# Performance work log

Hardware: AMD Instinct MI355X
Metric: run time of the kernel (lower is better)

Reference implementation:

```python
import jax, jax.numpy as jnp
import numpy as np

N = 4096          # num_nodes
F = 64            # node_features
H = 128           # hidden_dim
NH = 4            # num_heads
HD = H // NH      # per-head dim = 32
L = 3             # num_layers
C = 7             # num_classes
EDGE_P = 0.004    # ~16 avg degree


def setup_inputs() -> dict:
    key = jax.random.key(0)
    ks = jax.random.split(key, 20)
    g = lambda k, shape, fan_in: jax.random.normal(k, shape, jnp.float32) / np.sqrt(fan_in)
    x = jax.random.normal(ks[0], (N, F), jnp.float32)
    adj = (jax.random.uniform(ks[1], (N, N)) < EDGE_P).astype(jnp.float32)
    return {
        "x": x,
        "adj": adj,
        "enc_W": g(ks[2], (F, H), F), "enc_b": jnp.zeros((H,), jnp.float32),
        "gcn_W": g(ks[3], (L, H, H), H), "gcn_b": jnp.zeros((L, H), jnp.float32),
        "attn_W": g(ks[4], (L, NH, H, HD), H), "attn_Wb": jnp.zeros((L, NH, HD), jnp.float32),
        "attn_a": g(ks[5], (L, NH, 2 * HD), 2 * HD), "attn_ab": jnp.zeros((L, NH), jnp.float32),
        "cls_W1": g(ks[6], (H, H // 2), H), "cls_b1": jnp.zeros((H // 2,), jnp.float32),
        "cls_W2": g(ks[7], (H // 2, C), H // 2), "cls_b2": jnp.zeros((C,), jnp.float32),
        "con_W1": g(ks[8], (H, H // 2), H), "con_b1": jnp.zeros((H // 2,), jnp.float32),
        "con_W2": g(ks[9], (H // 2, 1), H // 2), "con_b2": jnp.zeros((1,), jnp.float32),
    }


def _normalize_adj(adj):
    a = adj + jnp.eye(adj.shape[0], dtype=adj.dtype)
    dinv = jnp.sum(a, axis=1) ** -0.5
    return dinv[:, None] * a * dinv[None, :]


def _gcn(h, adj_norm, W, b):
    support = adj_norm @ h                      # [N,H]
    return jax.nn.relu(support @ W + b)         # dropout=0 (eval)


def _attention(h, edge_mask, W, Wb, a, ab):
    # h:[N,H], W:[NH,H,HD], a:[NH,2*HD]; per-pair score = Linear(concat(h_i,h_j))
    hh = jnp.einsum('nf,hfd->hnd', h, W) + Wb[:, None, :]     # [NH,N,HD]
    a_src, a_dst = a[:, :HD], a[:, HD:]
    s_src = jnp.einsum('hnd,hd->hn', hh, a_src)               # [NH,N]
    s_dst = jnp.einsum('hnd,hd->hn', hh, a_dst)               # [NH,N]
    scores = s_src[:, :, None] + s_dst[:, None, :] + ab[:, None, None]
    # original uses literal 0.0 (NOT -inf) for non-edges before softmax
    scores = jnp.where(edge_mask[None, :, :], scores, 0.0)    # [NH,N,N]
    probs = jax.nn.softmax(scores, axis=-1)
    out = jnp.einsum('hij,hjd->hid', probs, hh)               # [NH,N,HD]
    return out.transpose(1, 0, 2).reshape(h.shape[0], NH * HD)


def reference(x, adj, enc_W, enc_b, gcn_W, gcn_b, attn_W, attn_Wb, attn_a, attn_ab,
              cls_W1, cls_b1, cls_W2, cls_b2, con_W1, con_b1, con_W2, con_b2):
    h = jax.nn.relu(x @ enc_W + enc_b)          # node encoder (dropout=0)
    adj_norm = _normalize_adj(adj)
    edge_mask = adj > 0
    for i in range(L):
        h_gcn = _gcn(h, adj_norm, gcn_W[i], gcn_b[i])
        h_attn = _attention(h, edge_mask, attn_W[i], attn_Wb[i], attn_a[i], attn_ab[i])
        h = jax.nn.relu(h_gcn + h_attn)
    node_logits = jax.nn.relu(h @ cls_W1 + cls_b1) @ cls_W2 + cls_b2
    h_mean = jnp.mean(h, axis=0, keepdims=True)
    contagion = jax.nn.relu(h_mean @ con_W1 + con_b1) @ con_W2 + con_b2
    return (node_logits, h, contagion)
```

## Files before the change

kernel.cpp:

```cpp
#include <hip/hip_runtime.h>

typedef unsigned short u16;
typedef unsigned int u32;

#define N 4096
#define F 64
#define H 128
#define NH 4
#define HD 32
#define EMAX 64

__device__ float g_hA[N * H];
__device__ float g_hB[N * H];
__device__ float g_hhA[N * H];
__device__ float g_hhB[N * H];
__device__ u16   g_cols[N * EMAX];
__device__ int   g_deg[N];
__device__ float g_dinv[N];
__device__ float g_ssrcA[N * NH];
__device__ float g_ssrcB[N * NH];
__device__ float g_sdstA[N * NH];
__device__ float g_sdstB[N * NH];
__device__ float g_part[3][32][H];
__device__ float g_hpart[32][H];

__global__ void k_csr(const float* __restrict__ adj) {
  __shared__ int cnt;
  int row = blockIdx.x;
  if (threadIdx.x == 0) cnt = 0;
  if (row == 0) {
    float* pz = &g_part[0][0][0];
    for (int i = threadIdx.x; i < 3 * 32 * H; i += 256) pz[i] = 0.f;
    float* hz = &g_hpart[0][0];
    for (int i = threadIdx.x; i < 32 * H; i += 256) hz[i] = 0.f;
  }
  __syncthreads();
  int base = threadIdx.x * 16;
  const float4* p = reinterpret_cast<const float4*>(adj + (size_t)row * N + base);
  float4 q0 = p[0], q1 = p[1], q2 = p[2], q3 = p[3];
  float vals[16] = {q0.x, q0.y, q0.z, q0.w, q1.x, q1.y, q1.z, q1.w,
                    q2.x, q2.y, q2.z, q2.w, q3.x, q3.y, q3.z, q3.w};
#pragma unroll
  for (int t = 0; t < 16; ++t)
    if (vals[t] != 0.f) {
      int pos = atomicAdd(&cnt, 1);
      if (pos < EMAX) g_cols[row * EMAX + pos] = (u16)(base + t);
    }
  __syncthreads();
  if (threadIdx.x == 0) {
    g_deg[row] = cnt < EMAX ? cnt : EMAX;
    g_dinv[row] = 1.0f / sqrtf((float)(cnt + 1));
  }
}

__device__ __forceinline__ void agg4(int i0, int tid, const float* __restrict__ h,
                                     const float* __restrict__ hhin,
                                     const float* __restrict__ ssrc_in,
                                     const float* __restrict__ sdst_in,
                                     int l, const float* __restrict__ abv,
                                     int (&jl)[4][EMAX], float (&dv)[4][EMAX],
                                     float (&sdl)[4][EMAX * NH],
                                     float& outa0, float& outa1,
                                     float& sup0, float& sup1) {
  int c = tid & 127, rg = tid >> 7, hc = c >> 5;
  int darr[4];
#pragma unroll
  for (int r = 0; r < 4; ++r) darr[r] = g_deg[i0 + r];
#pragma unroll
  for (int r = 0; r < 4; ++r) {
    const u16* cl = g_cols + (size_t)(i0 + r) * EMAX;
    for (int e = tid; e < darr[r]; e += 256) {
      int j = cl[e];
      jl[r][e] = j;
      dv[r][e] = g_dinv[j];
    }
  }
  __syncthreads();
#pragma unroll
  for (int r = 0; r < 4; ++r)
    for (int idx = tid; idx < darr[r] * NH; idx += 256)
      sdl[r][idx] = sdst_in[jl[r][idx >> 2] * NH + (idx & 3)];
  __syncthreads();

  float sumc = 0.f;
  const float* part = &g_part[l][0][0];
#pragma unroll
  for (int s = 0; s < 32; ++s) sumc += part[s * H + c];
  float ab = abv[hc];

  float oa[2], sp[2];
#pragma unroll
  for (int rr = 0; rr < 2; ++rr) {
    int r = rg * 2 + rr;
    int i = i0 + r, dd = darr[r];
    float ssrc = ssrc_in[i * NH + hc];
    float M = -INFINITY;
    for (int e = 0; e < dd; ++e) M = fmaxf(M, sdl[r][e * NH + hc]);
    float mv = fmaxf(0.f, ssrc + ab + M);
    float em = expf(-mv);
    float base = ssrc + ab - mv;
    float aA = 0.f, aT = 0.f, aG = 0.f, S = 0.f;
    int e = 0;
    for (; e + 2 <= dd; e += 2) {
      int j0 = jl[r][e], j1 = jl[r][e + 1];
      float q0 = hhin[j0 * H + c], q1 = hhin[j1 * H + c];
      float p0 = h[j0 * H + c], p1 = h[j1 * H + c];
      float w0 = expf(base + sdl[r][e * NH + hc]);
      float w1 = expf(base + sdl[r][(e + 1) * NH + hc]);
      aA = fmaf(w0, q0, aA); aA = fmaf(w1, q1, aA);
      aT += q0 + q1;
      aG = fmaf(dv[r][e], p0, aG); aG = fmaf(dv[r][e + 1], p1, aG);
      S += w0 + w1;
    }
    for (; e < dd; ++e) {
      int j = jl[r][e];
      float w = expf(base + sdl[r][e * NH + hc]);
      float q = hhin[j * H + c];
      aA = fmaf(w, q, aA);
      aT += q;
      aG = fmaf(dv[r][e], h[j * H + c], aG);
      S += w;
    }
    float Z = S + em * (float)(N - dd);
    oa[rr] = (aA + em * (sumc - aT)) / Z;
    float di = g_dinv[i];
    sp[rr] = di * (aG + di * h[i * H + c]);
  }
  outa0 = oa[0]; outa1 = oa[1]; sup0 = sp[0]; sup1 = sp[1];
}

__device__ __forceinline__ void proj4(int i0, int tid, const float (&hrowT)[H][4],
                                      const float* __restrict__ aW,
                                      const float* __restrict__ aWb,
                                      const float* __restrict__ aa, int lp,
                                      float* __restrict__ hhout,
                                      float* __restrict__ ssrc_out,
                                      float* __restrict__ sdst_out) {
  int c = tid & 127, rg = tid >> 7, hc = c >> 5, dc = c & 31;
  float b = aWb[hc * HD + dc];
  float p0 = b, p1 = b;
  for (int f = 0; f < H; ++f) {
    float w = aW[(hc * H + f) * HD + dc];
    float2 hv = *reinterpret_cast<const float2*>(&hrowT[f][rg * 2]);
    p0 = fmaf(hv.x, w, p0);
    p1 = fmaf(hv.y, w, p1);
  }
  int r0 = i0 + rg * 2, r1 = r0 + 1;
  hhout[r0 * H + c] = p0;
  hhout[r1 * H + c] = p1;
  const float* ap = aa + hc * 2 * HD;
  float as = ap[dc], ad = ap[HD + dc];
  float ss0 = p0 * as, ss1 = p1 * as, sd0 = p0 * ad, sd1 = p1 * ad;
#pragma unroll
  for (int m = 16; m >= 1; m >>= 1) {
    ss0 += __shfl_xor(ss0, m, 64); ss1 += __shfl_xor(ss1, m, 64);
    sd0 += __shfl_xor(sd0, m, 64); sd1 += __shfl_xor(sd1, m, 64);
  }
  if (dc == 0) {
    ssrc_out[r0 * NH + hc] = ss0; ssrc_out[r1 * NH + hc] = ss1;
    sdst_out[r0 * NH + hc] = sd0; sdst_out[r1 * NH + hc] = sd1;
  }
  atomicAdd(&g_part[lp][r0 & 31][c], p0);
  atomicAdd(&g_part[lp][r1 & 31][c], p1);
}

__global__ void k_enc_proj(const float* __restrict__ x, const float* __restrict__ eW,
                           const float* __restrict__ eb, const float* __restrict__ aW,
                           const float* __restrict__ aWb, const float* __restrict__ aa) {
  __shared__ float xT[F][4];
  __shared__ float hrowT[H][4];
  int i0 = blockIdx.x * 4, tid = threadIdx.x;
  int c = tid & 127, rg = tid >> 7;
  {
    int r = tid >> 6, k = tid & 63;
    xT[k][r] = x[(i0 + r) * F + k];
  }
  __syncthreads();
  float b = eb[c];
  float e0 = b, e1 = b;
  for (int k = 0; k < F; ++k) {
    float w = eW[k * H + c];
    float2 xv = *reinterpret_cast<const float2*>(&xT[k][rg * 2]);
    e0 = fmaf(xv.x, w, e0);
    e1 = fmaf(xv.y, w, e1);
  }
  e0 = fmaxf(e0, 0.f); e1 = fmaxf(e1, 0.f);
  int r0 = i0 + rg * 2, r1 = r0 + 1;
  g_hA[r0 * H + c] = e0; g_hA[r1 * H + c] = e1;
  hrowT[c][rg * 2] = e0; hrowT[c][rg * 2 + 1] = e1;
  __syncthreads();
  proj4(i0, tid, hrowT, aW, aWb, aa, 0, g_hhA, g_ssrcA, g_sdstA);
}

__global__ void k_acp(int pp, int l, const float* __restrict__ gW,
                      const float* __restrict__ gb, const float* __restrict__ aW,
                      const float* __restrict__ aWb, const float* __restrict__ aa,
                      const float* __restrict__ abv) {
  const float* h    = pp ? g_hB : g_hA;
  float*       hout = pp ? g_hA : g_hB;
  const float* hhin = pp ? g_hhB : g_hhA;
  float*       hhout= pp ? g_hhA : g_hhB;
  const float* ssin = pp ? g_ssrcB : g_ssrcA;
  float*       ssout= pp ? g_ssrcA : g_ssrcB;
  const float* sdin = pp ? g_sdstB : g_sdstA;
  float*       sdout= pp ? g_sdstA : g_sdstB;
  __shared__ int   jl[4][EMAX];
  __shared__ float dv[4][EMAX];
  __shared__ float sdl[4][EMAX * NH];
  __shared__ float srowT[H][4];
  __shared__ float hrowT[H][4];
  int i0 = blockIdx.x * 4, tid = threadIdx.x;
  int c = tid & 127, rg = tid >> 7;

  float oa0, oa1, sp0, sp1;
  agg4(i0, tid, h, hhin, ssin, sdin, l, abv, jl, dv, sdl, oa0, oa1, sp0, sp1);
  srowT[c][rg * 2] = sp0; srowT[c][rg * 2 + 1] = sp1;
  __syncthreads();

  float b = gb[c];
  float a0 = b, a1 = b;
  for (int f = 0; f < H; ++f) {
    float w = gW[f * H + c];
    float2 sv = *reinterpret_cast<const float2*>(&srowT[f][rg * 2]);
    a0 = fmaf(sv.x, w, a0);
    a1 = fmaf(sv.y, w, a1);
  }
  float g0 = fmaxf(fmaxf(a0, 0.f) + oa0, 0.f);
  float g1 = fmaxf(fmaxf(a1, 0.f) + oa1, 0.f);
  int r0 = i0 + rg * 2, r1 = r0 + 1;
  hout[r0 * H + c] = g0; hout[r1 * H + c] = g1;
  hrowT[c][rg * 2] = g0; hrowT[c][rg * 2 + 1] = g1;
  __syncthreads();

  proj4(i0, tid, hrowT, aW, aWb, aa, l + 1, hhout, ssout, sdout);
}

__global__ void k_acc(const float* __restrict__ abv, const float* __restrict__ gW,
                      const float* __restrict__ gb,
                      const float* __restrict__ W1, const float* __restrict__ b1,
                      const float* __restrict__ W2, const float* __restrict__ b2,
                      float* __restrict__ out, float* __restrict__ outh) {
  __shared__ int   jl[4][EMAX];
  __shared__ float dv[4][EMAX];
  __shared__ float sdl[4][EMAX * NH];
  __shared__ float srowT[H][4];
  __shared__ float hrowT[H][4];
  __shared__ float tl[4][64];
  int i0 = blockIdx.x * 4, tid = threadIdx.x;
  int c = tid & 127, rg = tid >> 7;

  float oa0, oa1, sp0, sp1;
  agg4(i0, tid, g_hA, g_hhA, g_ssrcA, g_sdstA, 2, abv, jl, dv, sdl, oa0, oa1, sp0, sp1);
  srowT[c][rg * 2] = sp0; srowT[c][rg * 2 + 1] = sp1;
  __syncthreads();

  float b = gb[c];
  float a0 = b, a1 = b;
  for (int f = 0; f < H; ++f) {
    float w = gW[f * H + c];
    float2 sv = *reinterpret_cast<const float2*>(&srowT[f][rg * 2]);
    a0 = fmaf(sv.x, w, a0);
    a1 = fmaf(sv.y, w, a1);
  }
  float g0 = fmaxf(fmaxf(a0, 0.f) + oa0, 0.f);
  float g1 = fmaxf(fmaxf(a1, 0.f) + oa1, 0.f);
  int r0 = i0 + rg * 2, r1 = r0 + 1;
  outh[r0 * H + c] = g0; outh[r1 * H + c] = g1;
  hrowT[c][rg * 2] = g0; hrowT[c][rg * 2 + 1] = g1;
  atomicAdd(&g_hpart[r0 & 31][c], g0);
  atomicAdd(&g_hpart[r1 & 31][c], g1);
  __syncthreads();

  int u = tid & 63, rr4 = tid >> 6;
  float a2 = b1[u];
  for (int f = 0; f < H; ++f) a2 = fmaf(hrowT[f][rr4], W1[f * 64 + u], a2);
  tl[rr4][u] = fmaxf(a2, 0.f);
  __syncthreads();
  if (tid < 28) {
    int r = tid / 7, j = tid - r * 7;
    float p = b2[j];
    for (int v = 0; v < 64; ++v) p = fmaf(tl[r][v], W2[v * 7 + j], p);
    out[(i0 + r) * 7 + j] = p;
  }
}

__global__ void k_contagion(const float* __restrict__ W1, const float* __restrict__ b1,
                            const float* __restrict__ W2, const float* __restrict__ b2,
                            float* __restrict__ out) {
  __shared__ float hm[H];
  __shared__ float tl[64];
  int u = threadIdx.x;
#pragma unroll
  for (int q = 0; q < 2; ++q) {
    int col = u + q * 64;
    float s = 0.f;
#pragma unroll
    for (int sl = 0; sl < 32; ++sl) s += g_hpart[sl][col];
    hm[col] = s * (1.0f / 4096.0f);
  }
  __syncthreads();
  float acc = b1[u];
  for (int f = 0; f < H; ++f) acc = fmaf(hm[f], W1[f * 64 + u], acc);
  tl[u] = fmaxf(acc, 0.f);
  __syncthreads();
  if (u == 0) {
    float p = b2[0];
    for (int v = 0; v < 64; ++v) p = fmaf(tl[v], W2[v], p);
    out[0] = p;
  }
}

extern "C" void kernel_launch(void* const* d_in, const int* in_sizes, int n_in,
                              void* d_out, int out_size, void* d_ws, size_t ws_size,
                              hipStream_t stream) {
  const float* x       = (const float*)d_in[0];
  const float* adj     = (const float*)d_in[1];
  const float* enc_W   = (const float*)d_in[2];
  const float* enc_b   = (const float*)d_in[3];
  const float* gcn_W   = (const float*)d_in[4];
  const float* gcn_b   = (const float*)d_in[5];
  const float* attn_W  = (const float*)d_in[6];
  const float* attn_Wb = (const float*)d_in[7];
  const float* attn_a  = (const float*)d_in[8];
  const float* attn_ab = (const float*)d_in[9];
  const float* cls_W1  = (const float*)d_in[10];
  const float* cls_b1  = (const float*)d_in[11];
  const float* cls_W2  = (const float*)d_in[12];
  const float* cls_b2  = (const float*)d_in[13];
  const float* con_W1  = (const float*)d_in[14];
  const float* con_b1  = (const float*)d_in[15];
  const float* con_W2  = (const float*)d_in[16];
  const float* con_b2  = (const float*)d_in[17];
  (void)in_sizes; (void)n_in; (void)d_ws; (void)ws_size; (void)out_size;

  float* out = (float*)d_out;
  float* outh = out + (size_t)N * 7;
  float* outc = out + (size_t)N * 7 + (size_t)N * H;

  k_csr<<<N, 256, 0, stream>>>(adj);
  k_enc_proj<<<N / 4, 256, 0, stream>>>(x, enc_W, enc_b, attn_W, attn_Wb, attn_a);
  k_acp<<<N / 4, 256, 0, stream>>>(0, 0, gcn_W, gcn_b,
                                   attn_W + (size_t)1 * NH * H * HD,
                                   attn_Wb + (size_t)1 * NH * HD,
                                   attn_a + (size_t)1 * NH * 2 * HD, attn_ab);
  k_acp<<<N / 4, 256, 0, stream>>>(1, 1, gcn_W + (size_t)1 * H * H, gcn_b + H,
                                   attn_W + (size_t)2 * NH * H * HD,
                                   attn_Wb + (size_t)2 * NH * HD,
                                   attn_a + (size_t)2 * NH * 2 * HD, attn_ab + NH);
  k_acc<<<N / 4, 256, 0, stream>>>(attn_ab + 2 * NH, gcn_W + (size_t)2 * H * H,
                                   gcn_b + 2 * H, cls_W1, cls_b1, cls_W2, cls_b2,
                                   out, outh);
  k_contagion<<<1, 64, 0, stream>>>(con_W1, con_b1, con_W2, con_b2, outc);
}
```

Before: 231.8 us.

## Fuse CSR build with encoder, pack h/hh, parallelize softmax, reduce atomics

Merges the CSR construction and encoder+projection into one launch with disjoint block ranges, and packs h and hh into a float2 array so each neighbour gather fetches both values in one load. The per-row max and softmax weights are now computed once per edge with wavefront shuffles and stored in shared memory, instead of each thread looping serially over all edges. Column-sum atomics are pre-reduced within the block and spread over 8 slots instead of 32, and the zeroing moves to a memset. The fused launch ties the encoder blocks to the CSR blocks' occupancy, and the extra memset and symbol lookup add host-side calls.

After: 278.8 us. 1.2x slower.

```diff
diff --git a/kernel.cpp b/kernel.cpp
--- a/kernel.cpp
+++ b/kernel.cpp
@@ -1,7 +1,6 @@
 #include <hip/hip_runtime.h>
 
 typedef unsigned short u16;
-typedef unsigned int u32;
 
 #define N 4096
 #define F 64
@@ -9,11 +8,10 @@
 #define NH 4
 #define HD 32
 #define EMAX 64
-
-__device__ float g_hA[N * H];
-__device__ float g_hB[N * H];
-__device__ float g_hhA[N * H];
-__device__ float g_hhB[N * H];
+#define NSLOT 8
+
+__device__ float2 g_pkA[N * H];
+__device__ float2 g_pkB[N * H];
 __device__ u16   g_cols[N * EMAX];
 __device__ int   g_deg[N];
 __device__ float g_dinv[N];
@@ -21,119 +19,15 @@
 __device__ float g_ssrcB[N * NH];
 __device__ float g_sdstA[N * NH];
 __device__ float g_sdstB[N * NH];
-__device__ float g_part[3][32][H];
-__device__ float g_hpart[32][H];
-
-__global__ void k_csr(const float* __restrict__ adj) {
-  __shared__ int cnt;
-  int row = blockIdx.x;
-  if (threadIdx.x == 0) cnt = 0;
-  if (row == 0) {
-    float* pz = &g_part[0][0][0];
-    for (int i = threadIdx.x; i < 3 * 32 * H; i += 256) pz[i] = 0.f;
-    float* hz = &g_hpart[0][0];
-    for (int i = threadIdx.x; i < 32 * H; i += 256) hz[i] = 0.f;
-  }
-  __syncthreads();
-  int base = threadIdx.x * 16;
-  const float4* p = reinterpret_cast<const float4*>(adj + (size_t)row * N + base);
-  float4 q0 = p[0], q1 = p[1], q2 = p[2], q3 = p[3];
-  float vals[16] = {q0.x, q0.y, q0.z, q0.w, q1.x, q1.y, q1.z, q1.w,
-                    q2.x, q2.y, q2.z, q2.w, q3.x, q3.y, q3.z, q3.w};
-#pragma unroll
-  for (int t = 0; t < 16; ++t)
-    if (vals[t] != 0.f) {
-      int pos = atomicAdd(&cnt, 1);
-      if (pos < EMAX) g_cols[row * EMAX + pos] = (u16)(base + t);
-    }
-  __syncthreads();
-  if (threadIdx.x == 0) {
-    g_deg[row] = cnt < EMAX ? cnt : EMAX;
-    g_dinv[row] = 1.0f / sqrtf((float)(cnt + 1));
-  }
-}
-
-__device__ __forceinline__ void agg4(int i0, int tid, const float* __restrict__ h,
-                                     const float* __restrict__ hhin,
-                                     const float* __restrict__ ssrc_in,
-                                     const float* __restrict__ sdst_in,
-                                     int l, const float* __restrict__ abv,
-                                     int (&jl)[4][EMAX], float (&dv)[4][EMAX],
-                                     float (&sdl)[4][EMAX * NH],
-                                     float& outa0, float& outa1,
-                                     float& sup0, float& sup1) {
-  int c = tid & 127, rg = tid >> 7, hc = c >> 5;
-  int darr[4];
-#pragma unroll
-  for (int r = 0; r < 4; ++r) darr[r] = g_deg[i0 + r];
-#pragma unroll
-  for (int r = 0; r < 4; ++r) {
-    const u16* cl = g_cols + (size_t)(i0 + r) * EMAX;
-    for (int e = tid; e < darr[r]; e += 256) {
-      int j = cl[e];
-      jl[r][e] = j;
-      dv[r][e] = g_dinv[j];
-    }
-  }
-  __syncthreads();
-#pragma unroll
-  for (int r = 0; r < 4; ++r)
-    for (int idx = tid; idx < darr[r] * NH; idx += 256)
-      sdl[r][idx] = sdst_in[jl[r][idx >> 2] * NH + (idx & 3)];
-  __syncthreads();
-
-  float sumc = 0.f;
-  const float* part = &g_part[l][0][0];
-#pragma unroll
-  for (int s = 0; s < 32; ++s) sumc += part[s * H + c];
-  float ab = abv[hc];
-
-  float oa[2], sp[2];
-#pragma unroll
-  for (int rr = 0; rr < 2; ++rr) {
-    int r = rg * 2 + rr;
-    int i = i0 + r, dd = darr[r];
-    float ssrc = ssrc_in[i * NH + hc];
-    float M = -INFINITY;
-    for (int e = 0; e < dd; ++e) M = fmaxf(M, sdl[r][e * NH + hc]);
-    float mv = fmaxf(0.f, ssrc + ab + M);
-    float em = expf(-mv);
-    float base = ssrc + ab - mv;
-    float aA = 0.f, aT = 0.f, aG = 0.f, S = 0.f;
-    int e = 0;
-    for (; e + 2 <= dd; e += 2) {
-      int j0 = jl[r][e], j1 = jl[r][e + 1];
-      float q0 = hhin[j0 * H + c], q1 = hhin[j1 * H + c];
-      float p0 = h[j0 * H + c], p1 = h[j1 * H + c];
-      float w0 = expf(base + sdl[r][e * NH + hc]);
-      float w1 = expf(base + sdl[r][(e + 1) * NH + hc]);
-      aA = fmaf(w0, q0, aA); aA = fmaf(w1, q1, aA);
-      aT += q0 + q1;
-      aG = fmaf(dv[r][e], p0, aG); aG = fmaf(dv[r][e + 1], p1, aG);
-      S += w0 + w1;
-    }
-    for (; e < dd; ++e) {
-      int j = jl[r][e];
-      float w = expf(base + sdl[r][e * NH + hc]);
-      float q = hhin[j * H + c];
-      aA = fmaf(w, q, aA);
-      aT += q;
-      aG = fmaf(dv[r][e], h[j * H + c], aG);
-      S += w;
-    }
-    float Z = S + em * (float)(N - dd);
-    oa[rr] = (aA + em * (sumc - aT)) / Z;
-    float di = g_dinv[i];
-    sp[rr] = di * (aG + di * h[i * H + c]);
-  }
-  outa0 = oa[0]; outa1 = oa[1]; sup0 = sp[0]; sup1 = sp[1];
-}
+__device__ float g_sumc[(3 + 1) * NSLOT * H];
 
 __device__ __forceinline__ void proj4(int i0, int tid, const float (&hrowT)[H][4],
                                       const float* __restrict__ aW,
                                       const float* __restrict__ aWb,
-                                      const float* __restrict__ aa, int lp,
-                                      float* __restrict__ hhout,
+                                      const float* __restrict__ aa,
+                                      float* __restrict__ sumcL, float (&csum)[H],
+                                      float hv0, float hv1,
+                                      float2* __restrict__ pkout,
                                       float* __restrict__ ssrc_out,
                                       float* __restrict__ sdst_out) {
   int c = tid & 127, rg = tid >> 7, hc = c >> 5, dc = c & 31;
@@ -146,8 +40,8 @@
     p1 = fmaf(hv.y, w, p1);
   }
   int r0 = i0 + rg * 2, r1 = r0 + 1;
-  hhout[r0 * H + c] = p0;
-  hhout[r1 * H + c] = p1;
+  pkout[(size_t)r0 * H + c] = make_float2(hv0, p0);
+  pkout[(size_t)r1 * H + c] = make_float2(hv1, p1);
   const float* ap = aa + hc * 2 * HD;
   float as = ap[dc], ad = ap[HD + dc];
   float ss0 = p0 * as, ss1 = p1 * as, sd0 = p0 * ad, sd1 = p1 * ad;
@@ -160,61 +54,188 @@
     ssrc_out[r0 * NH + hc] = ss0; ssrc_out[r1 * NH + hc] = ss1;
     sdst_out[r0 * NH + hc] = sd0; sdst_out[r1 * NH + hc] = sd1;
   }
-  atomicAdd(&g_part[lp][r0 & 31][c], p0);
-  atomicAdd(&g_part[lp][r1 & 31][c], p1);
-}
-
-__global__ void k_enc_proj(const float* __restrict__ x, const float* __restrict__ eW,
-                           const float* __restrict__ eb, const float* __restrict__ aW,
-                           const float* __restrict__ aWb, const float* __restrict__ aa) {
+  float psum = p0 + p1;
+  if (rg == 0) csum[c] = psum;
+  __syncthreads();
+  if (rg == 1) atomicAdd(&sumcL[(blockIdx.x & (NSLOT - 1)) * H + c], csum[c] + psum);
+}
+
+__device__ __forceinline__ void agg4(int i0, int tid, const float2* __restrict__ pk,
+                                     const float* __restrict__ ssin,
+                                     const float* __restrict__ sdin,
+                                     const float* __restrict__ sumcL,
+                                     const float* __restrict__ abv,
+                                     int (&jl)[4][EMAX], float (&dv)[4][EMAX],
+                                     float (&wl)[4][EMAX * NH],
+                                     float (&oa)[2], float (&sp)[2]) {
+  int c = tid & 127, rg = tid >> 7, hc = c >> 5, lg = tid & 31;
+  int4 dg = *reinterpret_cast<const int4*>(&g_deg[i0]);
+  const int* dga = reinterpret_cast<const int*>(&dg);
+#pragma unroll
+  for (int r = 0; r < 4; ++r) {
+    int dd = dga[r];
+    const u16* cl = g_cols + (size_t)(i0 + r) * EMAX;
+    for (int e = tid; e < dd; e += 256) {
+      int j = cl[e];
+      jl[r][e] = j;
+      dv[r][e] = g_dinv[j];
+    }
+  }
+  __syncthreads();
+
+  float em[2], Sv[2];
+#pragma unroll
+  for (int rr = 0; rr < 2; ++rr) {
+    int r = rg * 2 + rr;
+    int i = i0 + r, dd = dga[r];
+    float s0 = -INFINITY, s1 = -INFINITY;
+    if (lg < dd)      s0 = sdin[jl[r][lg] * NH + hc];
+    if (lg + 32 < dd) s1 = sdin[jl[r][lg + 32] * NH + hc];
+    float M = fmaxf(s0, s1);
+#pragma unroll
+    for (int m = 16; m >= 1; m >>= 1) M = fmaxf(M, __shfl_xor(M, m, 64));
+    float ssrc = ssin[i * NH + hc];
+    float ab = abv[hc];
+    float mv = fmaxf(0.f, ssrc + ab + M);
+    em[rr] = expf(-mv);
+    float base = ssrc + ab - mv;
+    float Sp = 0.f;
+    if (lg < dd) {
+      float w0 = expf(base + s0);
+      wl[r][lg * NH + hc] = w0;
+      Sp = w0;
+    }
+    if (lg + 32 < dd) {
+      float w1 = expf(base + s1);
+      wl[r][(lg + 32) * NH + hc] = w1;
+      Sp += w1;
+    }
+#pragma unroll
+    for (int m = 16; m >= 1; m >>= 1) Sp += __shfl_xor(Sp, m, 64);
+    Sv[rr] = Sp;
+  }
+  __syncthreads();
+
+  float sumc = 0.f;
+#pragma unroll
+  for (int s = 0; s < NSLOT; ++s) sumc += sumcL[s * H + c];
+
+  const float2* pkc = pk + c;
+#pragma unroll
+  for (int rr = 0; rr < 2; ++rr) {
+    int r = rg * 2 + rr;
+    int i = i0 + r, dd = dga[r];
+    float aA = 0.f, aT = 0.f, aG = 0.f;
+    int e = 0;
+    for (; e + 4 <= dd; e += 4) {
+      int j0 = jl[r][e],     j1 = jl[r][e + 1];
+      int j2 = jl[r][e + 2], j3 = jl[r][e + 3];
+      float2 q0 = pkc[(size_t)j0 * H], q1 = pkc[(size_t)j1 * H];
+      float2 q2 = pkc[(size_t)j2 * H], q3 = pkc[(size_t)j3 * H];
+      float w0 = wl[r][e * NH + hc],       w1 = wl[r][(e + 1) * NH + hc];
+      float w2 = wl[r][(e + 2) * NH + hc], w3 = wl[r][(e + 3) * NH + hc];
+      aA = fmaf(w0, q0.y, aA); aA = fmaf(w1, q1.y, aA);
+      aA = fmaf(w2, q2.y, aA); aA = fmaf(w3, q3.y, aA);
+      aT += (q0.y + q1.y) + (q2.y + q3.y);
+      aG = fmaf(dv[r][e], q0.x, aG);     aG = fmaf(dv[r][e + 1], q1.x, aG);
+      aG = fmaf(dv[r][e + 2], q2.x, aG); aG = fmaf(dv[r][e + 3], q3.x, aG);
+    }
+    for (; e < dd; ++e) {
+      int j = jl[r][e];
+      float2 q = pkc[(size_t)j * H];
+      float w = wl[r][e * NH + hc];
+      aA = fmaf(w, q.y, aA);
+      aT += q.y;
+      aG = fmaf(dv[r][e], q.x, aG);
+    }
+    float Z = Sv[rr] + em[rr] * (float)(N - dd);
+    float di = g_dinv[i];
+    oa[rr] = (aA + em[rr] * (sumc - aT)) / Z;
+    sp[rr] = di * (aG + di * pkc[(size_t)i * H].x);
+  }
+}
+
+__global__ __launch_bounds__(256, 4) void k_csr_enc(
+    const float* __restrict__ adj, const float* __restrict__ x,
+    const float* __restrict__ eW, const float* __restrict__ eb,
+    const float* __restrict__ aW, const float* __restrict__ aWb,
+    const float* __restrict__ aa) {
   __shared__ float xT[F][4];
   __shared__ float hrowT[H][4];
+  __shared__ float csum[H];
+  __shared__ int cnt;
+  int tid = threadIdx.x;
+  if (blockIdx.x < N / 4) {
+    int i0 = blockIdx.x * 4;
+    int c = tid & 127, rg = tid >> 7;
+    {
+      int r = tid >> 6, k = tid & 63;
+      xT[k][r] = x[(size_t)(i0 + r) * F + k];
+    }
+    __syncthreads();
+    float b = eb[c];
+    float e0 = b, e1 = b;
+    for (int k = 0; k < F; ++k) {
+      float w = eW[k * H + c];
+      float2 xv = *reinterpret_cast<const float2*>(&xT[k][rg * 2]);
+      e0 = fmaf(xv.x, w, e0);
+      e1 = fmaf(xv.y, w, e1);
+    }
+    e0 = fmaxf(e0, 0.f); e1 = fmaxf(e1, 0.f);
+    hrowT[c][rg * 2] = e0; hrowT[c][rg * 2 + 1] = e1;
+    __syncthreads();
+    proj4(i0, tid, hrowT, aW, aWb, aa, g_sumc, csum, e0, e1,
+          g_pkA, g_ssrcA, g_sdstA);
+  } else {
+    int row = blockIdx.x - N / 4;
+    if (tid == 0) cnt = 0;
+    __syncthreads();
+    const float* rp = adj + (size_t)row * N;
+    float4 q[4];
+#pragma unroll
+    for (int k2 = 0; k2 < 4; ++k2)
+      q[k2] = *reinterpret_cast<const float4*>(rp + k2 * 1024 + tid * 4);
+#pragma unroll
+    for (int k2 = 0; k2 < 4; ++k2) {
+      int base = k2 * 1024 + tid * 4;
+      float v[4] = {q[k2].x, q[k2].y, q[k2].z, q[k2].w};
+#pragma unroll
+      for (int t = 0; t < 4; ++t)
+        if (v[t] != 0.f) {
+          int pos = atomicAdd(&cnt, 1);
+          if (pos < EMAX) g_cols[row * EMAX + pos] = (u16)(base + t);
+        }
+    }
+    __syncthreads();
+    if (tid == 0) {
+      g_deg[row] = cnt < EMAX ? cnt : EMAX;
+      g_dinv[row] = 1.0f / sqrtf((float)(cnt + 1));
+    }
+  }
+}
+
+__global__ __launch_bounds__(256, 4) void k_acp(
+    int pp, int l, const float* __restrict__ gW, const float* __restrict__ gb,
+    const float* __restrict__ aW, const float* __restrict__ aWb,
+    const float* __restrict__ aa, const float* __restrict__ abv) {
+  const float2* pk    = pp ? g_pkB : g_pkA;
+  float2*       pkout = pp ? g_pkA : g_pkB;
+  const float*  ssin  = pp ? g_ssrcB : g_ssrcA;
+  float*        ssout = pp ? g_ssrcA : g_ssrcB;
+  const float*  sdin  = pp ? g_sdstB : g_sdstA;
+  float*        sdout = pp ? g_sdstA : g_sdstB;
+  __shared__ int   jl[4][EMAX];
+  __shared__ float dv[4][EMAX];
+  __shared__ float wl[4][EMAX * NH];
+  __shared__ float srowT[H][4];
+  __shared__ float hrowT[H][4];
+  __shared__ float csum[H];
   int i0 = blockIdx.x * 4, tid = threadIdx.x;
   int c = tid & 127, rg = tid >> 7;
-  {
-    int r = tid >> 6, k = tid & 63;
-    xT[k][r] = x[(i0 + r) * F + k];
-  }
-  __syncthreads();
-  float b = eb[c];
-  float e0 = b, e1 = b;
-  for (int k = 0; k < F; ++k) {
-    float w = eW[k * H + c];
-    float2 xv = *reinterpret_cast<const float2*>(&xT[k][rg * 2]);
-    e0 = fmaf(xv.x, w, e0);
-    e1 = fmaf(xv.y, w, e1);
-  }
-  e0 = fmaxf(e0, 0.f); e1 = fmaxf(e1, 0.f);
-  int r0 = i0 + rg * 2, r1 = r0 + 1;
-  g_hA[r0 * H + c] = e0; g_hA[r1 * H + c] = e1;
-  hrowT[c][rg * 2] = e0; hrowT[c][rg * 2 + 1] = e1;
-  __syncthreads();
-  proj4(i0, tid, hrowT, aW, aWb, aa, 0, g_hhA, g_ssrcA, g_sdstA);
-}
-
-__global__ void k_acp(int pp, int l, const float* __restrict__ gW,
-                      const float* __restrict__ gb, const float* __restrict__ aW,
-                      const float* __restrict__ aWb, const float* __restrict__ aa,
-                      const float* __restrict__ abv) {
-  const float* h    = pp ? g_hB : g_hA;
-  float*       hout = pp ? g_hA : g_hB;
-  const float* hhin = pp ? g_hhB : g_hhA;
-  float*       hhout= pp ? g_hhA : g_hhB;
-  const float* ssin = pp ? g_ssrcB : g_ssrcA;
-  float*       ssout= pp ? g_ssrcA : g_ssrcB;
-  const float* sdin = pp ? g_sdstB : g_sdstA;
-  float*       sdout= pp ? g_sdstA : g_sdstB;
-  __shared__ int   jl[4][EMAX];
-  __shared__ float dv[4][EMAX];
-  __shared__ float sdl[4][EMAX * NH];
-  __shared__ float srowT[H][4];
-  __shared__ float hrowT[H][4];
-  int i0 = blockIdx.x * 4, tid = threadIdx.x;
-  int c = tid & 127, rg = tid >> 7;
-
-  float oa0, oa1, sp0, sp1;
-  agg4(i0, tid, h, hhin, ssin, sdin, l, abv, jl, dv, sdl, oa0, oa1, sp0, sp1);
-  srowT[c][rg * 2] = sp0; srowT[c][rg * 2 + 1] = sp1;
+
+  float oa[2], sp[2];
+  agg4(i0, tid, pk, ssin, sdin, g_sumc + l * NSLOT * H, abv, jl, dv, wl, oa, sp);
+  srowT[c][rg * 2] = sp[0]; srowT[c][rg * 2 + 1] = sp[1];
   __syncthreads();
 
   float b = gb[c];
@@ -225,33 +246,35 @@
     a0 = fmaf(sv.x, w, a0);
     a1 = fmaf(sv.y, w, a1);
   }
-  float g0 = fmaxf(fmaxf(a0, 0.f) + oa0, 0.f);
-  float g1 = fmaxf(fmaxf(a1, 0.f) + oa1, 0.f);
-  int r0 = i0 + rg * 2, r1 = r0 + 1;
-  hout[r0 * H + c] = g0; hout[r1 * H + c] = g1;
+  float g0 = fmaxf(fmaxf(a0, 0.f) + oa[0], 0.f);
+  float g1 = fmaxf(fmaxf(a1, 0.f) + oa[1], 0.f);
   hrowT[c][rg * 2] = g0; hrowT[c][rg * 2 + 1] = g1;
   __syncthreads();
 
-  proj4(i0, tid, hrowT, aW, aWb, aa, l + 1, hhout, ssout, sdout);
-}
-
-__global__ void k_acc(const float* __restrict__ abv, const float* __restrict__ gW,
-                      const float* __restrict__ gb,
-                      const float* __restrict__ W1, const float* __restrict__ b1,
-                      const float* __restrict__ W2, const float* __restrict__ b2,
-                      float* __restrict__ out, float* __restrict__ outh) {
+  proj4(i0, tid, hrowT, aW, aWb, aa, g_sumc + (l + 1) * NSLOT * H, csum,
+        g0, g1, pkout, ssout, sdout);
+}
+
+__global__ __launch_bounds__(256, 4) void k_acc(
+    const float* __restrict__ abv, const float* __restrict__ gW,
+    const float* __restrict__ gb,
+    const float* __restrict__ W1, const float* __restrict__ b1,
+    const float* __restrict__ W2, const float* __restrict__ b2,
+    float* __restrict__ out, float* __restrict__ outh) {
   __shared__ int   jl[4][EMAX];
   __shared__ float dv[4][EMAX];
-  __shared__ float sdl[4][EMAX * NH];
+  __shared__ float wl[4][EMAX * NH];
   __shared__ float srowT[H][4];
   __shared__ float hrowT[H][4];
+  __shared__ float csum[H];
   __shared__ float tl[4][64];
   int i0 = blockIdx.x * 4, tid = threadIdx.x;
   int c = tid & 127, rg = tid >> 7;
 
-  float oa0, oa1, sp0, sp1;
-  agg4(i0, tid, g_hA, g_hhA, g_ssrcA, g_sdstA, 2, abv, jl, dv, sdl, oa0, oa1, sp0, sp1);
-  srowT[c][rg * 2] = sp0; srowT[c][rg * 2 + 1] = sp1;
+  float oa[2], sp[2];
+  agg4(i0, tid, g_pkA, g_ssrcA, g_sdstA, g_sumc + 2 * NSLOT * H, abv,
+       jl, dv, wl, oa, sp);
+  srowT[c][rg * 2] = sp[0]; srowT[c][rg * 2 + 1] = sp[1];
   __syncthreads();
 
   float b = gb[c];
@@ -262,14 +285,18 @@
     a0 = fmaf(sv.x, w, a0);
     a1 = fmaf(sv.y, w, a1);
   }
-  float g0 = fmaxf(fmaxf(a0, 0.f) + oa0, 0.f);
-  float g1 = fmaxf(fmaxf(a1, 0.f) + oa1, 0.f);
+  float g0 = fmaxf(fmaxf(a0, 0.f) + oa[0], 0.f);
+  float g1 = fmaxf(fmaxf(a1, 0.f) + oa[1], 0.f);
   int r0 = i0 + rg * 2, r1 = r0 + 1;
-  outh[r0 * H + c] = g0; outh[r1 * H + c] = g1;
+  outh[(size_t)r0 * H + c] = g0;
+  outh[(size_t)r1 * H + c] = g1;
   hrowT[c][rg * 2] = g0; hrowT[c][rg * 2 + 1] = g1;
-  atomicAdd(&g_hpart[r0 & 31][c], g0);
-  atomicAdd(&g_hpart[r1 & 31][c], g1);
-  __syncthreads();
+  float gsum = g0 + g1;
+  if (rg == 0) csum[c] = gsum;
+  __syncthreads();
+  if (rg == 1)
+    atomicAdd(&g_sumc[3 * NSLOT * H + (blockIdx.x & (NSLOT - 1)) * H + c],
+              csum[c] + gsum);
 
   int u = tid & 63, rr4 = tid >> 6;
   float a2 = b1[u];
@@ -280,7 +307,7 @@
     int r = tid / 7, j = tid - r * 7;
     float p = b2[j];
     for (int v = 0; v < 64; ++v) p = fmaf(tl[r][v], W2[v * 7 + j], p);
-    out[(i0 + r) * 7 + j] = p;
+    out[(size_t)(i0 + r) * 7 + j] = p;
   }
 }
 
@@ -290,12 +317,13 @@
   __shared__ float hm[H];
   __shared__ float tl[64];
   int u = threadIdx.x;
+  const float* hp = g_sumc + 3 * NSLOT * H;
 #pragma unroll
   for (int q = 0; q < 2; ++q) {
     int col = u + q * 64;
     float s = 0.f;
 #pragma unroll
-    for (int sl = 0; sl < 32; ++sl) s += g_hpart[sl][col];
+    for (int sl = 0; sl < NSLOT; ++sl) s += hp[sl * H + col];
     hm[col] = s * (1.0f / 4096.0f);
   }
   __syncthreads();
@@ -337,8 +365,12 @@
   float* outh = out + (size_t)N * 7;
   float* outc = out + (size_t)N * 7 + (size_t)N * H;
 
-  k_csr<<<N, 256, 0, stream>>>(adj);
-  k_enc_proj<<<N / 4, 256, 0, stream>>>(x, enc_W, enc_b, attn_W, attn_Wb, attn_a);
+  void* zr = nullptr;
+  hipGetSymbolAddress(&zr, HIP_SYMBOL(g_sumc));
+  hipMemsetAsync(zr, 0, sizeof(float) * (3 + 1) * NSLOT * H, stream);
+
+  k_csr_enc<<<N / 4 + N, 256, 0, stream>>>(adj, x, enc_W, enc_b,
+                                           attn_W, attn_Wb, attn_a);
   k_acp<<<N / 4, 256, 0, stream>>>(0, 0, gcn_W, gcn_b,
                                    attn_W + (size_t)1 * NH * H * HD,
                                    attn_Wb + (size_t)1 * NH * HD,
```
